# Kernel optimization log

Hardware: AMD Instinct MI355X
Metric: run time of the kernel (lower is better)

## Reference

```python
import jax, jax.numpy as jnp
import numpy as np
from jax import lax

B, S, K, E, H, V = 32, 160, 44, 300, 256, 32000


def _gru_dir(x, Wih, Whh, bih, bhh, reverse=False):
    # x: [N, T, D] -> (outputs [N, T, H], final hidden [N, H]); PyTorch GRU cell math
    def step(h, xt):
        gi = xt @ Wih.T + bih
        gh = h @ Whh.T + bhh
        ir, iz, inn = jnp.split(gi, 3, axis=-1)
        hr, hz, hn = jnp.split(gh, 3, axis=-1)
        r = jax.nn.sigmoid(ir + hr)
        z = jax.nn.sigmoid(iz + hz)
        n = jnp.tanh(inn + r * hn)
        h_new = (1.0 - z) * n + z * h
        return h_new, h_new

    xs = jnp.swapaxes(x, 0, 1)  # [T, N, D]
    if reverse:
        xs = xs[::-1]
    h0 = jnp.zeros((x.shape[0], Whh.shape[1]), x.dtype)
    hT, hs = lax.scan(step, h0, xs)
    if reverse:
        hs = hs[::-1]
    return jnp.swapaxes(hs, 0, 1), hT


def _bigru(x, p):
    of, hf = _gru_dir(x, p['Wif'], p['Whf'], p['bif'], p['bhf'])
    ob, hb = _gru_dir(x, p['Wib'], p['Whb'], p['bib'], p['bhb'], reverse=True)
    return jnp.concatenate([of, ob], axis=-1), hf, hb


def setup_inputs() -> dict:
    key = jax.random.key(0)
    ks = jax.random.split(key, 32)

    def n(k, shape, s=0.05):
        return jax.random.normal(k, shape, jnp.float32) * s

    inp = {}
    inp['x1'] = jax.random.randint(ks[0], (B, S), 0, V, dtype=jnp.int32)
    inp['x2'] = jax.random.randint(ks[1], (B, S), 0, V, dtype=jnp.int32)
    inp['keys_c'] = jax.random.randint(ks[2], (B, S, K), 0, V, dtype=jnp.int32)
    inp['keys_r'] = jax.random.randint(ks[3], (B, S, K), 0, V, dtype=jnp.int32)
    inp['x1mask'] = jnp.ones((B, S), jnp.float32)
    inp['emb'] = n(ks[4], (V, E))
    # key-embedding bidirectional GRU (input dim E)
    inp['kWif'] = n(ks[5], (3 * H, E)); inp['kWhf'] = n(ks[6], (3 * H, H))
    inp['kbif'] = n(ks[7], (3 * H,));  inp['kbhf'] = n(ks[8], (3 * H,))
    inp['kWib'] = n(ks[9], (3 * H, E)); inp['kWhb'] = n(ks[10], (3 * H, H))
    inp['kbib'] = n(ks[11], (3 * H,)); inp['kbhb'] = n(ks[12], (3 * H,))
    # encoder bidirectional GRU (input dim E + H: word emb concat key emb)
    inp['eWif'] = n(ks[13], (3 * H, E + H)); inp['eWhf'] = n(ks[14], (3 * H, H))
    inp['ebif'] = n(ks[15], (3 * H,));       inp['ebhf'] = n(ks[16], (3 * H,))
    inp['eWib'] = n(ks[17], (3 * H, E + H)); inp['eWhb'] = n(ks[18], (3 * H, H))
    inp['ebib'] = n(ks[19], (3 * H,));       inp['ebhb'] = n(ks[20], (3 * H,))
    # bilinear attention + output bilinear
    inp['attn_W'] = n(ks[21], (2 * H, 2 * H)); inp['attn_b'] = n(ks[22], (2 * H,))
    inp['M'] = n(ks[23], (2 * H, 2 * H));      inp['b'] = jnp.zeros((1,), jnp.float32)
    return inp


def reference(x1, x2, keys_c, keys_r, x1mask, emb,
              kWif, kWhf, kbif, kbhf, kWib, kWhb, kbib, kbhb,
              eWif, eWhf, ebif, ebhf, eWib, eWhb, ebib, ebhb,
              attn_W, attn_b, M, b):
    kp = dict(Wif=kWif, Whf=kWhf, bif=kbif, bhf=kbhf, Wib=kWib, Whb=kWhb, bib=kbib, bhb=kbhb)
    ep = dict(Wif=eWif, Whf=eWhf, bif=ebif, bhf=ebhf, Wib=eWib, Whb=eWhb, bib=ebib, bhb=ebhb)

    # Per-position key GRU embedding: original loops a full nn.GRU over every
    # sequence position; here we collapse to ONE batched pass over B*S sequences.
    def key_emb(keys):
        ke = emb[keys.reshape(B * S, K)]          # [B*S, K, E]
        _, hf, hb = _bigru(ke, kp)
        return (hf + hb).reshape(B, S, H)         # combine directions -> h_dim slot

    kc = key_emb(keys_c)
    kr = key_emb(keys_r)

    # encoder (dropout is identity in eval)
    x1e = jnp.concatenate([emb[x1], kc], axis=-1)  # [B, S, E+H]
    x2e = jnp.concatenate([emb[x2], kr], axis=-1)
    sc, c1f, c1b = _bigru(x1e, ep)                 # sc: [B, S, 2H]
    _, r1f, r1b = _bigru(x2e, ep)
    r = jnp.concatenate([r1f, r1b], axis=-1)       # [B, 2H]

    # bilinear attention of response final state over context states
    a = sc @ attn_W.T + attn_b                     # [B, S, 2H]
    energies = jnp.einsum('bsd,bd->bs', a, r)
    alpha = jax.nn.softmax(energies, axis=-1) * x1mask
    c_attn = jnp.einsum('bs,bsd->bd', alpha, sc)   # [B, 2H]

    # final bilinear score
    o = jnp.einsum('bd,de,be->b', c_attn, M, r) + b[0]
    return o
```

## Files before the change

### kernel.cpp

```cpp
#include <hip/hip_runtime.h>
#include <hip/hip_bf16.h>

#define BB 32
#define SS 160
#define KK 44
#define EE 300
#define HH 256
#define VV 32000
#define G3 768
#define EHP 576
#define EP  320
#define NSEQ 5120
#define NROW 10240
#define NKEY 20480

typedef unsigned short u16;
typedef unsigned char u8;
typedef long i64;
typedef __attribute__((ext_vector_type(8))) short bf16x8;
typedef __attribute__((ext_vector_type(4))) float f32x4;
typedef __attribute__((ext_vector_type(2))) float f32x2;
typedef __attribute__((ext_vector_type(4))) int i32x4;

static __device__ __forceinline__ u16 f2bf(float f) {
  union { float f; unsigned u; } x; x.f = f;
  unsigned u = x.u;
  unsigned r = (u + 0x7fffu + ((u >> 16) & 1u)) >> 16;
  return (u16)r;
}
static __device__ __forceinline__ float bf2f(u16 v) {
  union { unsigned u; float f; } x; x.u = ((unsigned)v) << 16;
  return x.f;
}
static __device__ __forceinline__ u8 ftofp8(float v) {
  return (u8)(__builtin_amdgcn_cvt_pk_fp8_f32(v, v, 0, false) & 0xff);
}
static __device__ __forceinline__ float fsig(float x) {
  float e = __expf(-x);
  return __builtin_amdgcn_rcpf(1.f + e);
}
static __device__ __forceinline__ float ftanh(float x) {
  float e = __expf(2.f * x);
  return 1.f - 2.f * __builtin_amdgcn_rcpf(1.f + e);
}

__global__ void cvt_pad(const float* __restrict__ src, u16* __restrict__ dst,
                        int rows, int K, int ldp) {
  int idx = blockIdx.x * blockDim.x + threadIdx.x;
  int tot = rows * ldp;
  if (idx >= tot) return;
  int c = idx % ldp; int r = idx / ldp;
  float v = (c < K) ? src[(size_t)r * K + c] : 0.f;
  dst[idx] = f2bf(v);
}

__global__ void cvt_f8(const float* __restrict__ src, u8* __restrict__ dst, int n) {
  int i = blockIdx.x * blockDim.x + threadIdx.x;
  if (i < n) dst[i] = ftofp8(src[i]);
}

__global__ void bias_comb(const float* __restrict__ bi, const float* __restrict__ bh,
                          float* __restrict__ o) {
  int j = blockIdx.x * blockDim.x + threadIdx.x;
  if (j >= G3) return;
  o[j] = bi[j] + (j < 512 ? bh[j] : 0.f);
}

__global__ void gemm_bt24(const u16* __restrict__ A, const u16* __restrict__ B,
                          float* __restrict__ C, u16* __restrict__ Cbf,
                          u8* __restrict__ C8,
                          const float* __restrict__ bias,
                          int M, int N, int K, int lda, int ldb, int ldc) {
  int gid = blockIdx.x * blockDim.x + threadIdx.x;
  int wid = gid >> 6, lane = gid & 63;
  int ntg = N >> 6;
  int total = (M >> 5) * ntg;
  if (wid >= total) return;
  int tm = wid / ntg, tg = wid - tm * ntg;
  int rbase = tm << 5, cbase = tg << 6;
  int m = lane & 15, quad = lane >> 4;
  const u16* ap0 = A + (size_t)(rbase + m) * lda + quad * 8;
  const u16* ap1 = ap0 + (size_t)16 * lda;
  const u16* bp0 = B + (size_t)(cbase + m) * ldb + quad * 8;
  f32x4 acc[2][4];
  #pragma unroll
  for (int r = 0; r < 2; ++r)
    #pragma unroll
    for (int c = 0; c < 4; ++c) acc[r][c] = (f32x4){0.f, 0.f, 0.f, 0.f};
  for (int k = 0; k < K; k += 32) {
    bf16x8 a0 = *(const bf16x8*)(ap0 + k);
    bf16x8 a1 = *(const bf16x8*)(ap1 + k);
    #pragma unroll
    for (int c = 0; c < 4; ++c) {
      bf16x8 bv = *(const bf16x8*)(bp0 + (size_t)c * 16 * ldb + k);
      acc[0][c] = __builtin_amdgcn_mfma_f32_16x16x32_bf16(a0, bv, acc[0][c], 0, 0, 0);
      acc[1][c] = __builtin_amdgcn_mfma_f32_16x16x32_bf16(a1, bv, acc[1][c], 0, 0, 0);
    }
  }
  #pragma unroll
  for (int c = 0; c < 4; ++c) {
    int col = cbase + c * 16 + m;
    float bv = bias ? bias[col] : 0.f;
    int g = col >> 8, cc = col & 255;
    #pragma unroll
    for (int rt = 0; rt < 2; ++rt) {
      int orow = rbase + rt * 16 + quad * 4;
      #pragma unroll
      for (int i = 0; i < 4; ++i) {
        float v = acc[rt][c][i] + bv;
        if (C8) {
          size_t rb = (size_t)(orow + i) * 1024;
          if (g < 2) C8[rb + 2 * cc + g] = ftofp8(v);
          else *(u16*)&C8[rb + 512 + 2 * cc] = f2bf(v);
        } else if (Cbf) Cbf[(size_t)(orow + i) * ldc + col] = f2bf(v);
        else C[(size_t)(orow + i) * ldc + col] = v;
      }
    }
  }
}

#define GLD16(gsrc, ldst)                                                     \
  __builtin_amdgcn_global_load_lds(                                           \
      (const __attribute__((address_space(1))) void*)(gsrc),                  \
      (__attribute__((address_space(3))) void*)(ldst), 16, 0, 0)

__global__ __launch_bounds__(1024) void key_gru16(
    const u8* __restrict__ W8f, const u8* __restrict__ W8b,
    const float* __restrict__ nbf, const float* __restrict__ nbb,
    const u8* __restrict__ T8F, const u8* __restrict__ T8B,
    const int* __restrict__ keys_c, const int* __restrict__ keys_r,
    float* __restrict__ h_out) {
  __shared__ __align__(16) u8 hb8[2][80 * 256];
  __shared__ __align__(16) u8 giL[6 * 16384];
  __shared__ int tokL[80 * KK];
  int b = blockIdx.x;
  int xcd = b & 7, slot0 = b >> 3;
  int bwd = xcd >> 2;
  int j = slot0 * 4 + (xcd & 3);
  int isR = j >> 6;
  int seq0 = (j & 63) * 80;
  const u8* W8 = bwd ? W8b : W8f;
  const u8* T = bwd ? T8B : T8F;
  const int* keys = isR ? keys_r : keys_c;
  const float* nb = bwd ? nbb : nbf;

  int tid = threadIdx.x;
  int w = tid >> 6, lane = tid & 63, m = lane & 15, quad = lane >> 4;
  int c = w * 16 + m;
  float nbv = nb[512 + c];

  for (int i = tid; i < 80 * KK; i += 1024)
    tokL[i] = keys[seq0 * KK + i];

  i64 w_r[8], w_z[8], w_n[8];
  {
    const u8* br = W8 + (size_t)(0 * 256 + c) * 256 + quad * 8;
    const u8* bz = W8 + (size_t)(1 * 256 + c) * 256 + quad * 8;
    const u8* bn = W8 + (size_t)(2 * 256 + c) * 256 + quad * 8;
    #pragma unroll
    for (int kc = 0; kc < 8; ++kc) {
      w_r[kc] = *(const i64*)(br + kc * 32);
      w_z[kc] = *(const i64*)(bz + kc * 32);
      w_n[kc] = *(const i64*)(bn + kc * 32);
    }
  }

  auto dma_grp = [&](int tt, int g, int sl) {
    int row = g * 16 + w;
    int tok = tokL[row * KK + tt];
    const u8* src = T + (size_t)tok * 1024 + lane * 16;
    u8* dst = giL + sl * 16384 + w * 1024;
    GLD16(src, dst);
  };

  for (int i = tid * 16; i < 80 * 256; i += 1024 * 16)
    *(i32x4*)&hb8[0][i] = (i32x4){0, 0, 0, 0};
  float h[5][4];
  #pragma unroll
  for (int rt = 0; rt < 5; ++rt)
    #pragma unroll
    for (int i = 0; i < 4; ++i) h[rt][i] = 0.f;

  asm volatile("s_waitcnt vmcnt(0) lgkmcnt(0)" ::: "memory");
  __builtin_amdgcn_s_barrier();

  {
    int t0 = bwd ? (KK - 1) : 0;
    #pragma unroll
    for (int g = 0; g < 5; ++g) dma_grp(t0, g, g);
  }

  int cc = c >> 3, lo = c & 7;
  int sb = 0;

  for (int step = 0; step < KK; ++step) {
    const u8* cur = hb8[step & 1];
    u8* nxt = hb8[(step & 1) ^ 1];
    int tnext = bwd ? (KK - 2 - step) : (step + 1);
    int tclamp = tnext < 0 ? 0 : (tnext > KK - 1 ? KK - 1 : tnext);

    #pragma unroll
    for (int rt = 0; rt < 5; ++rt) {
      f32x4 acc[3];
      #pragma unroll
      for (int g = 0; g < 3; ++g) acc[g] = (f32x4){0.f, 0.f, 0.f, 0.f};
      int arow = rt * 16 + m;
      #pragma unroll
      for (int kc = 0; kc < 8; ++kc) {
        i64 a = *(const i64*)&cur[arow * 256 + (((quad + 4 * kc) ^ (arow & 31)) * 8)];
        acc[0] = __builtin_amdgcn_mfma_f32_16x16x32_fp8_fp8(a, w_r[kc], acc[0], 0, 0, 0);
        acc[1] = __builtin_amdgcn_mfma_f32_16x16x32_fp8_fp8(a, w_z[kc], acc[1], 0, 0, 0);
        acc[2] = __builtin_amdgcn_mfma_f32_16x16x32_fp8_fp8(a, w_n[kc], acc[2], 0, 0, 0);
      }

      asm volatile("s_waitcnt vmcnt(4)" ::: "memory");
      __builtin_amdgcn_s_barrier();
      __builtin_amdgcn_sched_barrier(0);

      const u16* giU = (const u16*)(giL + ((rt + sb) % 6) * 16384);
      #pragma unroll
      for (int i = 0; i < 4; ++i) {
        int lrow = quad * 4 + i;
        int row = rt * 16 + lrow;
        u16 vrz = giU[lrow * 512 + c];
        f32x2 grz = __builtin_amdgcn_cvt_pk_f32_fp8((int)vrz, false);
        float gn = bf2f(giU[lrow * 512 + 256 + c]);
        float rr = fsig(grz[0] + acc[0][i]);
        float zz = fsig(grz[1] + acc[1][i]);
        float nn = ftanh(gn + rr * (acc[2][i] + nbv));
        float hv = (1.f - zz) * nn + zz * h[rt][i];
        h[rt][i] = hv;
        nxt[row * 256 + ((cc ^ (row & 31)) * 8) + lo] = ftofp8(hv);
      }
      __builtin_amdgcn_sched_barrier(0);
      dma_grp(tclamp, rt, (rt + sb + 5) % 6);
    }

    asm volatile("s_waitcnt lgkmcnt(0)" ::: "memory");
    __builtin_amdgcn_s_barrier();
    sb = (sb + 5) % 6;
  }

  __syncthreads();
  float* hstage = (float*)giL;
  #pragma unroll
  for (int rt = 0; rt < 5; ++rt)
    #pragma unroll
    for (int i = 0; i < 4; ++i)
      hstage[(rt * 16 + quad * 4 + i) * 256 + c] = h[rt][i];
  __syncthreads();
  size_t rowbase = (size_t)(bwd * NROW + isR * NSEQ + seq0) * 256;
  for (int i = tid * 4; i < 80 * 256; i += 1024 * 4)
    *(f32x4*)&h_out[rowbase + i] = *(const f32x4*)&hstage[i];
}

__global__ void build_xe(const float* __restrict__ emb, const int* __restrict__ x1,
                         const int* __restrict__ x2, const float* __restrict__ hk,
                         u16* __restrict__ xe) {
  int idx = blockIdx.x * blockDim.x + threadIdx.x;
  if (idx >= NROW * EHP) return;
  int c = idx % EHP; int rr = idx / EHP;
  int isX2 = rr >= NSEQ;
  int seq = rr - (isX2 ? NSEQ : 0);
  float v;
  if (c < EE) {
    int tok = (isX2 ? x2 : x1)[seq];
    v = emb[(size_t)tok * EE + c];
  } else if (c < EE + HH) {
    int j = c - EE;
    int frow = (isX2 ? NSEQ : 0) + seq;
    v = hk[(size_t)frow * HH + j] + hk[(size_t)(NROW + frow) * HH + j];
  } else {
    v = 0.f;
  }
  xe[idx] = f2bf(v);
}

__global__ __launch_bounds__(1024, 1) void main_gru4(
    const u16* __restrict__ Wf, const u16* __restrict__ Wb,
    const float* __restrict__ nbf, const float* __restrict__ nbb,
    const float* __restrict__ Gf, const float* __restrict__ Gb,
    float* __restrict__ sc, u16* __restrict__ scbf,
    float* __restrict__ rvec, u16* __restrict__ rbf) {
  __shared__ __align__(16) u16 hbuf[2][16 * 256];
  int rt = blockIdx.x;
  int q = rt >> 1;
  int bwd = q >> 1, isX2 = q & 1;
  const u16* W = bwd ? Wb : Wf;
  const float* G = bwd ? Gb : Gf;
  const float* nb = bwd ? nbb : nbf;
  int tid = threadIdx.x, w = tid >> 6, lane = tid & 63, m = lane & 15, quad = lane >> 4;
  int c = w * 16 + m;
  float nbv = nb[512 + c];

  const u16* bp[3];
  #pragma unroll
  for (int g = 0; g < 3; ++g)
    bp[g] = W + (size_t)(g * 256 + c) * 256 + quad * 8;

  for (int i = tid * 8; i < 16 * 256; i += 1024 * 8)
    *(i32x4*)&hbuf[0][i] = (i32x4){0, 0, 0, 0};
  float h[4];
  #pragma unroll
  for (int i = 0; i < 4; ++i) h[i] = 0.f;
  __syncthreads();

  for (int step = 0; step < SS; ++step) {
    const u16* cur = hbuf[step & 1];
    u16* nxt = hbuf[(step & 1) ^ 1];
    int s = bwd ? (SS - 1 - step) : step;
    float gi[3][4];
    #pragma unroll
    for (int i = 0; i < 4; ++i) {
      int bb = ((rt & 1) << 4) + quad * 4 + i;
      size_t girow = ((size_t)(isX2 * NSEQ + bb * SS + s)) * G3;
      #pragma unroll
      for (int g = 0; g < 3; ++g)
        gi[g][i] = G[girow + g * 256 + c];
    }
    f32x4 acc[3];
    #pragma unroll
    for (int g = 0; g < 3; ++g) acc[g] = (f32x4){0.f, 0.f, 0.f, 0.f};
    #pragma unroll
    for (int k = 0; k < 8; ++k) {
      bf16x8 a = *(const bf16x8*)&cur[m * 256 + (((quad + 4 * k) ^ m) * 8)];
      #pragma unroll
      for (int g = 0; g < 3; ++g) {
        bf16x8 bv = *(const bf16x8*)(bp[g] + k * 32);
        acc[g] = __builtin_amdgcn_mfma_f32_16x16x32_bf16(a, bv, acc[g], 0, 0, 0);
      }
    }
    int cc = c >> 3, lo = c & 7;
    #pragma unroll
    for (int i = 0; i < 4; ++i) {
      int row_l = quad * 4 + i;
      float rr = fsig(gi[0][i] + acc[0][i]);
      float zz = fsig(gi[1][i] + acc[1][i]);
      float nn = ftanh(gi[2][i] + rr * (acc[2][i] + nbv));
      float hv = (1.f - zz) * nn + zz * h[i];
      h[i] = hv;
      nxt[row_l * 256 + ((cc ^ row_l) * 8) + lo] = f2bf(hv);
      if (!isX2) {
        int bb = ((rt & 1) << 4) + row_l;
        size_t o = (size_t)(bb * SS + s) * 512 + (bwd ? 256 : 0) + c;
        sc[o] = hv;
        scbf[o] = f2bf(hv);
      }
    }
    __syncthreads();
  }
  if (isX2) {
    #pragma unroll
    for (int i = 0; i < 4; ++i) {
      int bb = ((rt & 1) << 4) + quad * 4 + i;
      size_t o = (size_t)bb * 512 + (bwd ? 256 : 0) + c;
      rvec[o] = h[i];
      rbf[o] = f2bf(h[i]);
    }
  }
}

__global__ void energies_k(const float* __restrict__ a, const float* __restrict__ r,
                           float* __restrict__ e) {
  int gid = blockIdx.x * blockDim.x + threadIdx.x;
  int wid = gid >> 6, lane = gid & 63;
  if (wid >= NSEQ) return;
  int b = wid / SS;
  const float* ar = a + (size_t)wid * 512;
  const float* rr = r + (size_t)b * 512;
  float sum = 0.f;
  for (int i = lane; i < 512; i += 64) sum += ar[i] * rr[i];
  for (int off = 32; off > 0; off >>= 1) sum += __shfl_down(sum, off);
  if (lane == 0) e[wid] = sum;
}

__global__ void softmax_k(const float* __restrict__ e, const float* __restrict__ mask,
                          float* __restrict__ alpha) {
  __shared__ float red[256];
  int b = blockIdx.x, tid = threadIdx.x;
  float v = (tid < SS) ? e[b * SS + tid] : -1e30f;
  red[tid] = v; __syncthreads();
  for (int s = 128; s > 0; s >>= 1) { if (tid < s) red[tid] = fmaxf(red[tid], red[tid + s]); __syncthreads(); }
  float mx = red[0]; __syncthreads();
  float ex = (tid < SS) ? expf(v - mx) : 0.f;
  red[tid] = ex; __syncthreads();
  for (int s = 128; s > 0; s >>= 1) { if (tid < s) red[tid] += red[tid + s]; __syncthreads(); }
  float denom = red[0];
  if (tid < SS) alpha[b * SS + tid] = ex / denom * mask[b * SS + tid];
}

__global__ void cattn_k(const float* __restrict__ alpha, const float* __restrict__ sc,
                        float* __restrict__ c) {
  int b = blockIdx.x, d = threadIdx.x;
  float sum = 0.f;
  for (int s = 0; s < SS; ++s)
    sum += alpha[b * SS + s] * sc[(size_t)(b * SS + s) * 512 + d];
  c[b * 512 + d] = sum;
}

__global__ void final_dot(const float* __restrict__ c, const float* __restrict__ v,
                          const float* __restrict__ bsc, float* __restrict__ out) {
  int b = blockIdx.x, lane = threadIdx.x;
  float s = 0.f;
  for (int i = lane; i < 512; i += 64) s += c[b * 512 + i] * v[b * 512 + i];
  for (int off = 32; off > 0; off >>= 1) s += __shfl_down(s, off);
  if (lane == 0) out[b] = s + bsc[0];
}

extern "C" void kernel_launch(void* const* d_in, const int* in_sizes, int n_in,
                              void* d_out, int out_size, void* d_ws, size_t ws_size,
                              hipStream_t stream) {
  const int*   x1     = (const int*)d_in[0];
  const int*   x2     = (const int*)d_in[1];
  const int*   keys_c = (const int*)d_in[2];
  const int*   keys_r = (const int*)d_in[3];
  const float* x1mask = (const float*)d_in[4];
  const float* emb    = (const float*)d_in[5];
  const float* kWif   = (const float*)d_in[6];
  const float* kWhf   = (const float*)d_in[7];
  const float* kbif   = (const float*)d_in[8];
  const float* kbhf   = (const float*)d_in[9];
  const float* kWib   = (const float*)d_in[10];
  const float* kWhb   = (const float*)d_in[11];
  const float* kbib   = (const float*)d_in[12];
  const float* kbhb   = (const float*)d_in[13];
  const float* eWif   = (const float*)d_in[14];
  const float* eWhf   = (const float*)d_in[15];
  const float* ebif   = (const float*)d_in[16];
  const float* ebhf   = (const float*)d_in[17];
  const float* eWib   = (const float*)d_in[18];
  const float* eWhb   = (const float*)d_in[19];
  const float* ebib   = (const float*)d_in[20];
  const float* ebhb   = (const float*)d_in[21];
  const float* attnW  = (const float*)d_in[22];
  const float* attnb  = (const float*)d_in[23];
  const float* Mw     = (const float*)d_in[24];
  const float* bsc    = (const float*)d_in[25];
  float* out = (float*)d_out;

  char* base = (char*)d_ws;
  size_t off = 0;
  auto take = [&](size_t bytes) -> void* {
    void* p = base + off; off += (bytes + 255) & ~(size_t)255; return p;
  };

  u16* kWif_bf = (u16*)take((size_t)G3 * EP * 2);
  u16* kWib_bf = (u16*)take((size_t)G3 * EP * 2);
  u8*  kW8f    = (u8*)take((size_t)G3 * HH);
  u8*  kW8b    = (u8*)take((size_t)G3 * HH);
  u16* eWif_bf = (u16*)take((size_t)G3 * EHP * 2);
  u16* eWib_bf = (u16*)take((size_t)G3 * EHP * 2);
  u16* eWhf_bf = (u16*)take((size_t)G3 * HH * 2);
  u16* eWhb_bf = (u16*)take((size_t)G3 * HH * 2);
  u16* attnW_bf = (u16*)take((size_t)512 * 512 * 2);
  u16* M_bf    = (u16*)take((size_t)512 * 512 * 2);
  u16* xe_bf   = (u16*)take((size_t)NROW * EHP * 2);
  float* cb_kf = (float*)take(G3 * 4);
  float* cb_kb = (float*)take(G3 * 4);
  float* cb_ef = (float*)take(G3 * 4);
  float* cb_eb = (float*)take(G3 * 4);
  float* h_key = (float*)take((size_t)NKEY * HH * 4);

  size_t pbase = off;
  u16* emb_bf = (u16*)take((size_t)VV * EP * 2);
  u8*  T8F    = (u8*)take((size_t)VV * 1024);
  u8*  T8B    = (u8*)take((size_t)VV * 1024);

  off = pbase;
  float* Gf = (float*)take((size_t)NROW * G3 * 4);
  float* Gb = (float*)take((size_t)NROW * G3 * 4);
  float* sc = (float*)take((size_t)NSEQ * 512 * 4);
  u16*   sc_bf = (u16*)take((size_t)NSEQ * 512 * 2);
  float* rvec = (float*)take((size_t)BB * 512 * 4);
  u16*   r_bf = (u16*)take((size_t)BB * 512 * 2);
  float* abuf = (float*)take((size_t)NSEQ * 512 * 4);
  float* energ = (float*)take((size_t)BB * SS * 4);
  float* alpha = (float*)take((size_t)BB * SS * 4);
  float* c_attn = (float*)take((size_t)BB * 512 * 4);
  float* vbuf = (float*)take((size_t)BB * 512 * 4);

  auto cvt = [&](const float* s, u16* d, int rows, int K, int ldp) {
    int tot = rows * ldp;
    cvt_pad<<<(tot + 255) / 256, 256, 0, stream>>>(s, d, rows, K, ldp);
  };
  auto gemm = [&](const u16* A, const u16* B, float* C, u16* Cbf, u8* C8,
                  const float* bias,
                  int M, int N, int K, int lda, int ldb, int ldc) {
    long long waves = (long long)(M >> 5) * (N >> 6);
    int blocks = (int)((waves * 64 + 255) / 256);
    gemm_bt24<<<blocks, 256, 0, stream>>>(A, B, C, Cbf, C8, bias, M, N, K, lda, ldb, ldc);
  };

  cvt(emb, emb_bf, VV, EE, EP);
  cvt(kWif, kWif_bf, G3, EE, EP);
  cvt(kWib, kWib_bf, G3, EE, EP);
  cvt_f8<<<(G3 * HH + 255) / 256, 256, 0, stream>>>(kWhf, kW8f, G3 * HH);
  cvt_f8<<<(G3 * HH + 255) / 256, 256, 0, stream>>>(kWhb, kW8b, G3 * HH);
  cvt(eWif, eWif_bf, G3, 556, EHP);
  cvt(eWib, eWib_bf, G3, 556, EHP);
  cvt(eWhf, eWhf_bf, G3, HH, HH);
  cvt(eWhb, eWhb_bf, G3, HH, HH);
  cvt(attnW, attnW_bf, 512, 512, 512);
  cvt(Mw, M_bf, 512, 512, 512);
  bias_comb<<<3, 256, 0, stream>>>(kbif, kbhf, cb_kf);
  bias_comb<<<3, 256, 0, stream>>>(kbib, kbhb, cb_kb);
  bias_comb<<<3, 256, 0, stream>>>(ebif, ebhf, cb_ef);
  bias_comb<<<3, 256, 0, stream>>>(ebib, ebhb, cb_eb);

  gemm(emb_bf, kWif_bf, nullptr, nullptr, T8F, cb_kf, VV, G3, EP, EP, EP, G3);
  gemm(emb_bf, kWib_bf, nullptr, nullptr, T8B, cb_kb, VV, G3, EP, EP, EP, G3);

  key_gru16<<<256, 1024, 0, stream>>>(kW8f, kW8b, kbhf, kbhb,
                                      T8F, T8B, keys_c, keys_r, h_key);

  build_xe<<<(NROW * EHP + 255) / 256, 256, 0, stream>>>(emb, x1, x2, h_key, xe_bf);

  gemm(xe_bf, eWif_bf, Gf, nullptr, nullptr, cb_ef, NROW, G3, EHP, EHP, EHP, G3);
  gemm(xe_bf, eWib_bf, Gb, nullptr, nullptr, cb_eb, NROW, G3, EHP, EHP, EHP, G3);

  main_gru4<<<8, 1024, 0, stream>>>(eWhf_bf, eWhb_bf, ebhf, ebhb,
                                    Gf, Gb, sc, sc_bf, rvec, r_bf);

  gemm(sc_bf, attnW_bf, abuf, nullptr, nullptr, attnb, NSEQ, 512, 512, 512, 512, 512);
  energies_k<<<(NSEQ * 64 + 255) / 256, 256, 0, stream>>>(abuf, rvec, energ);
  softmax_k<<<BB, 256, 0, stream>>>(energ, x1mask, alpha);
  cattn_k<<<BB, 512, 0, stream>>>(alpha, sc, c_attn);
  gemm(r_bf, M_bf, vbuf, nullptr, nullptr, nullptr, BB, 512, 512, 512, 512, 512);
  final_dot<<<BB, 64, 0, stream>>>(c_attn, vbuf, bsc, out);
}
```

Before: 1.901 ms.

## Prefetch next-step GRU input gates into LDS via async DMA in main GRU

The main encoder GRU loop now issues asynchronous global-to-LDS loads (GLD16) of the next timestep's precomputed input-gate rows into a double-buffered shared array. The loads overlap with the current step's MFMA recurrence, replacing the scattered per-thread global reads that sat on the serial critical path. Synchronisation is now done with explicit waitcnt and s_barrier calls instead of __syncthreads. This adds 96KB of LDS and relies on correct vmcnt accounting; a wrong count could race with the DMA.

```diff
diff --git a/kernel.cpp b/kernel.cpp
--- a/kernel.cpp
+++ b/kernel.cpp
@@ -276,13 +276,14 @@
   xe[idx] = f2bf(v);
 }
 
-__global__ __launch_bounds__(1024, 1) void main_gru4(
+__global__ __launch_bounds__(1024, 1) void main_gru6(
     const u16* __restrict__ Wf, const u16* __restrict__ Wb,
     const float* __restrict__ nbf, const float* __restrict__ nbb,
     const float* __restrict__ Gf, const float* __restrict__ Gb,
     float* __restrict__ sc, u16* __restrict__ scbf,
     float* __restrict__ rvec, u16* __restrict__ rbf) {
   __shared__ __align__(16) u16 hbuf[2][16 * 256];
+  __shared__ __align__(16) u8 giB[2][16 * 3072];
   int rt = blockIdx.x;
   int q = rt >> 1;
   int bwd = q >> 1, isX2 = q & 1;
@@ -298,26 +299,34 @@
   for (int g = 0; g < 3; ++g)
     bp[g] = W + (size_t)(g * 256 + c) * 256 + quad * 8;
 
+  auto dma_gi = [&](int s, int buf) {
+    size_t rowbase = ((size_t)(isX2 * NSEQ + (((rt & 1) << 4) + w) * SS + s)) * G3;
+    const u8* src = (const u8*)(G + rowbase) + lane * 16;
+    u8* dst = giB[buf] + w * 3072;
+    #pragma unroll
+    for (int ch = 0; ch < 3; ++ch)
+      GLD16(src + ch * 1024, dst + ch * 1024);
+  };
+
   for (int i = tid * 8; i < 16 * 256; i += 1024 * 8)
     *(i32x4*)&hbuf[0][i] = (i32x4){0, 0, 0, 0};
   float h[4];
   #pragma unroll
   for (int i = 0; i < 4; ++i) h[i] = 0.f;
-  __syncthreads();
+
+  dma_gi(bwd ? (SS - 1) : 0, 0);
+  asm volatile("s_waitcnt vmcnt(0) lgkmcnt(0)" ::: "memory");
+  __builtin_amdgcn_s_barrier();
 
   for (int step = 0; step < SS; ++step) {
     const u16* cur = hbuf[step & 1];
     u16* nxt = hbuf[(step & 1) ^ 1];
     int s = bwd ? (SS - 1 - step) : step;
-    float gi[3][4];
-    #pragma unroll
-    for (int i = 0; i < 4; ++i) {
-      int bb = ((rt & 1) << 4) + quad * 4 + i;
-      size_t girow = ((size_t)(isX2 * NSEQ + bb * SS + s)) * G3;
-      #pragma unroll
-      for (int g = 0; g < 3; ++g)
-        gi[g][i] = G[girow + g * 256 + c];
-    }
+    int sn = bwd ? (SS - 2 - step) : (step + 1);
+    int snc = sn < 0 ? 0 : (sn > SS - 1 ? SS - 1 : sn);
+
+    dma_gi(snc, (step & 1) ^ 1);
+
     f32x4 acc[3];
     #pragma unroll
     for (int g = 0; g < 3; ++g) acc[g] = (f32x4){0.f, 0.f, 0.f, 0.f};
@@ -330,24 +339,36 @@
         acc[g] = __builtin_amdgcn_mfma_f32_16x16x32_bf16(a, bv, acc[g], 0, 0, 0);
       }
     }
+
+    asm volatile("s_waitcnt vmcnt(3)" ::: "memory");
+    __builtin_amdgcn_s_barrier();
+    __builtin_amdgcn_sched_barrier(0);
+
+    const u8* giC = giB[step & 1];
     int cc = c >> 3, lo = c & 7;
     #pragma unroll
     for (int i = 0; i < 4; ++i) {
-      int row_l = quad * 4 + i;
-      float rr = fsig(gi[0][i] + acc[0][i]);
-      float zz = fsig(gi[1][i] + acc[1][i]);
-      float nn = ftanh(gi[2][i] + rr * (acc[2][i] + nbv));
+      int r = quad * 4 + i;
+      const float* gr = (const float*)(giC + r * 3072);
+      float g0 = gr[0 * 256 + c];
+      float g1 = gr[1 * 256 + c];
+      float g2 = gr[2 * 256 + c];
+      float rr = fsig(g0 + acc[0][i]);
+      float zz = fsig(g1 + acc[1][i]);
+      float nn = ftanh(g2 + rr * (acc[2][i] + nbv));
       float hv = (1.f - zz) * nn + zz * h[i];
       h[i] = hv;
-      nxt[row_l * 256 + ((cc ^ row_l) * 8) + lo] = f2bf(hv);
+      nxt[r * 256 + ((cc ^ r) * 8) + lo] = f2bf(hv);
       if (!isX2) {
-        int bb = ((rt & 1) << 4) + row_l;
+        int bb = ((rt & 1) << 4) + r;
         size_t o = (size_t)(bb * SS + s) * 512 + (bwd ? 256 : 0) + c;
         sc[o] = hv;
         scbf[o] = f2bf(hv);
       }
     }
-    __syncthreads();
+
+    asm volatile("s_waitcnt lgkmcnt(0)" ::: "memory");
+    __builtin_amdgcn_s_barrier();
   }
   if (isX2) {
     #pragma unroll
@@ -518,7 +539,7 @@
   gemm(xe_bf, eWif_bf, Gf, nullptr, nullptr, cb_ef, NROW, G3, EHP, EHP, EHP, G3);
   gemm(xe_bf, eWib_bf, Gb, nullptr, nullptr, cb_eb, NROW, G3, EHP, EHP, EHP, G3);
 
-  main_gru4<<<8, 1024, 0, stream>>>(eWhf_bf, eWhb_bf, ebhf, ebhb,
+  main_gru6<<<8, 1024, 0, stream>>>(eWhf_bf, eWhb_bf, ebhf, ebhb,
                                     Gf, Gb, sc, sc_bf, rvec, r_bf);
 
   gemm(sc_bf, attnW_bf, abuf, nullptr, nullptr, attnb, NSEQ, 512, 512, 512, 512, 512);
```

After: 1.958 ms. 3.0% more time.
